# Kernel tuning notes

Hardware: AMD Instinct MI355X
Metric: run time of the kernel (lower is better)

Reference implementation:

```python
import jax, jax.numpy as jnp
import numpy as np

B, L, N, D, H, E = 16, 3, 512, 1024, 4096, 3


def setup_inputs() -> dict:
    key = jax.random.key(0)
    ks = jax.random.split(key, 6)
    tensors = jax.random.normal(ks[0], (B, L, N, D), jnp.float32)
    mask = jax.random.bernoulli(ks[1], 0.3, (B, L, N))  # True = padded
    wg = jax.random.normal(ks[2], (D, E), jnp.float32) * 0.02   # gate (Linear, no bias)
    We = jax.random.normal(ks[3], (E, D, D), jnp.float32) * 0.02  # per-expert Linear weight
    be = jnp.zeros((E, D), jnp.float32)                          # per-expert Linear bias
    Wp = jax.random.normal(ks[4], (D, H), jnp.float32) * 0.02    # GAP head projector
    bp = jnp.zeros((H,), jnp.float32)
    return dict(tensors=tensors, mask=mask, wg=wg, We=We, be=be, Wp=Wp, bp=bp)


def _moe_top1(x, wg, We, be):
    # x: [S, D]. DeepSpeed-style top-1 gating with capacity_factor=1.
    S, d = x.shape
    n_exp = wg.shape[1]
    cap = -(-S // n_exp)  # ceil(S / E) * capacity_factor(=1)
    gates = jax.nn.softmax(x @ wg, axis=-1)              # [S, E]
    idx = jnp.argmax(gates, axis=-1)                      # [S]
    m1 = jax.nn.one_hot(idx, n_exp, dtype=jnp.int32)      # [S, E]
    me = gates.mean(axis=0)
    ce = m1.astype(gates.dtype).mean(axis=0)
    l_aux = jnp.sum(me * ce) * n_exp                      # aux load-balancing loss
    # position of each token within its expert's buffer (arrival order)
    loc = jnp.cumsum(m1, axis=0) - 1                      # [S, E]
    loc_s = jnp.sum(loc * m1, axis=-1)                    # [S]
    keep = (loc_s < cap).astype(x.dtype)                  # drop overflow tokens
    gate_s = jnp.sum(gates * m1.astype(gates.dtype), axis=-1) * keep
    loc_c = jnp.minimum(loc_s, cap - 1)
    # dispatch (scatter), grouped GEMM per expert, combine (gather)
    disp = jnp.zeros((n_exp, cap, d), x.dtype).at[idx, loc_c].add(x * keep[:, None])
    eo = jnp.einsum('ecd,edh->ech', disp, We) + be[:, None, :]
    y = eo[idx, loc_c] * gate_s[:, None]                  # [S, D]
    return y, l_aux


def reference(tensors, mask, wg, We, be, Wp, bp):
    b, l, n, d = tensors.shape
    # permute(0,2,1,3).reshape(B*N, L, D) then flatten tokens
    x = tensors.transpose(0, 2, 1, 3).reshape(b * n * l, d)
    y, l_aux = _moe_top1(x, wg, We, be)
    y = y.reshape(b, n, l, d).transpose(0, 2, 1, 3)       # back to [B, L, N, D]
    # GAP head: projector then masked mean pool (sum over ALL tokens,
    # divided by non-masked count, matching the source exactly)
    p = y @ Wp + bp                                       # [B, L, N, H]
    p = p.reshape(b, l * n, -1)
    m = mask.reshape(b, l * n)
    s = p.sum(axis=1)                                     # [B, H]
    cnt = jnp.clip(jnp.sum(~m, axis=1, keepdims=True), 1, None).astype(p.dtype)
    return s / cnt, l_aux
```

## Files before the change

### kernel.cpp

```cpp
#include <hip/hip_runtime.h>
#include <hip/hip_bf16.h>
#include <cstdint>

#define LL 3
#define NN 512
#define DD 1024
#define HH 4096
#define SS 24576
#define LNTOK 1536
#define CAP 8192

#define OFF_HIST    0
#define OFF_GSUM    640
#define OFF_GBE     704
#define OFF_CNTI    768
#define OFF_NDROP   832
#define OFF_Z       960
#define OFF_YS      50112
#define OFF_ZEROEND 66496
#define OFF_IDX     66496
#define OFF_GVAL    91072
#define OFF_DROP    115648
#define OFF_END     132032
#define OFF_PZ      132032
#define OFF_PP      656320
#define OFF_YS2     1704896
#define OFF_BIG_END 1721280

__global__ __launch_bounds__(256) void k0_mask(const void* __restrict__ maskp,
                                               int* __restrict__ cnti) {
  __shared__ int det;
  __shared__ int scnt;
  int tid = threadIdx.x;
  if (tid == 0) { det = 0; scnt = 0; }
  __syncthreads();
  const uint32_t* mw = (const uint32_t*)maskp;
  for (int i = tid; i < LNTOK; i += 256) {
    uint32_t v = mw[i];
    if (v == 0x3F800000u) det = 2;
    else if (v > 1u) det = 1;
  }
  __syncthreads();
  int t = blockIdx.x * 256 + tid;
  int zero;
  if (det == 1) zero = (((const uint8_t*)maskp)[t] == 0);
  else          zero = (mw[t] == 0);
  unsigned long long bal = __ballot(zero);
  if ((tid & 63) == 0) atomicAdd(&scnt, __popcll(bal));
  __syncthreads();
  if (tid == 0) atomicAdd(&cnti[blockIdx.x / 6], scnt);
}

__global__ __launch_bounds__(256, 4) void k1_gate(const float* __restrict__ x,
                                                  const float* __restrict__ wg,
                                                  int* __restrict__ idx,
                                                  float* __restrict__ gval,
                                                  int* __restrict__ hist,
                                                  float* __restrict__ gsum,
                                                  float* __restrict__ gbe) {
  __shared__ float wgT[3][1024];
  __shared__ float part[16 * 195];
  __shared__ float sd[48];
  __shared__ float sG[3], sB[3];
  __shared__ int   sH[3];
  int tid = threadIdx.x, lane = tid & 63, w = tid >> 6;
  for (int i = tid; i < 3072; i += 256) wgT[i % 3][i / 3] = wg[i];
  if (tid < 3) { sG[tid] = 0.f; sB[tid] = 0.f; sH[tid] = 0; }
  __syncthreads();
  int dd = lane * 4;
  float4 W[12];
#pragma unroll
  for (int e = 0; e < 3; ++e)
#pragma unroll
    for (int q = 0; q < 4; ++q)
      W[e * 4 + q] = *(const float4*)(&wgT[e][dd + q * 256]);
  int t0 = blockIdx.x * 16;
  int b = t0 / LNTOK;
  int r0 = t0 % LNTOK;

#pragma unroll
  for (int k = 0; k < 4; ++k) {
    int tok = w * 4 + k;
    int r = r0 + tok;
    int n = r / LL, l = r % LL;
    const float* row = x + (size_t)((b * LL + l) * NN + n) * DD + dd;
    float4 v0 = *(const float4*)(row);
    float4 v1 = *(const float4*)(row + 256);
    float4 v2 = *(const float4*)(row + 512);
    float4 v3 = *(const float4*)(row + 768);
    float d0 = v0.x * W[0].x + v0.y * W[0].y + v0.z * W[0].z + v0.w * W[0].w +
               v1.x * W[1].x + v1.y * W[1].y + v1.z * W[1].z + v1.w * W[1].w +
               v2.x * W[2].x + v2.y * W[2].y + v2.z * W[2].z + v2.w * W[2].w +
               v3.x * W[3].x + v3.y * W[3].y + v3.z * W[3].z + v3.w * W[3].w;
    float d1 = v0.x * W[4].x + v0.y * W[4].y + v0.z * W[4].z + v0.w * W[4].w +
               v1.x * W[5].x + v1.y * W[5].y + v1.z * W[5].z + v1.w * W[5].w +
               v2.x * W[6].x + v2.y * W[6].y + v2.z * W[6].z + v2.w * W[6].w +
               v3.x * W[7].x + v3.y * W[7].y + v3.z * W[7].z + v3.w * W[7].w;
    float d2 = v0.x * W[8].x + v0.y * W[8].y + v0.z * W[8].z + v0.w * W[8].w +
               v1.x * W[9].x + v1.y * W[9].y + v1.z * W[9].z + v1.w * W[9].w +
               v2.x * W[10].x + v2.y * W[10].y + v2.z * W[10].z + v2.w * W[10].w +
               v3.x * W[11].x + v3.y * W[11].y + v3.z * W[11].z + v3.w * W[11].w;
    part[tok * 195 + lane] = d0;
    part[tok * 195 + 65 + lane] = d1;
    part[tok * 195 + 130 + lane] = d2;
  }
  __syncthreads();

  if (tid < 48) {
    const float* p = part + tid * 65;
    float s0 = 0, s1 = 0, s2 = 0, s3 = 0;
#pragma unroll
    for (int l = 0; l < 64; l += 4) {
      s0 += p[l]; s1 += p[l + 1]; s2 += p[l + 2]; s3 += p[l + 3];
    }
    sd[tid] = (s0 + s1) + (s2 + s3);
  }
  __syncthreads();

  if (tid < 16) {
    float d0 = sd[tid * 3], d1 = sd[tid * 3 + 1], d2 = sd[tid * 3 + 2];
    float m = d0; int id = 0;
    if (d1 > m) { m = d1; id = 1; }
    if (d2 > m) { m = d2; id = 2; }
    float e0 = expf(d0 - m), e1 = expf(d1 - m), e2 = expf(d2 - m);
    float inv = 1.0f / (e0 + e1 + e2);
    int t = t0 + tid;
    idx[t] = id;
    gval[t] = inv;
    atomicAdd(&sG[0], e0 * inv);
    atomicAdd(&sG[1], e1 * inv);
    atomicAdd(&sG[2], e2 * inv);
    atomicAdd(&sB[id], inv);
    atomicAdd(&sH[id], 1);
  }
  __syncthreads();
  if (tid < 3) {
    atomicAdd(&gsum[tid], sG[tid]);
    atomicAdd(&gbe[b * 3 + tid], sB[tid]);
    atomicAdd(&hist[(blockIdx.x >> 4) * 3 + tid], sH[tid]);
  }
}

__global__ __launch_bounds__(256, 4) void k2_zacc(const float* __restrict__ x,
                                                  const int* __restrict__ idx,
                                                  const float* __restrict__ gval,
                                                  float* __restrict__ z) {
  __shared__ float sg[384];
  __shared__ int   se[384];
  __shared__ float pacc[4][3][64];
  int tid = threadIdx.x;
  int blk = blockIdx.x;
  int b = blk >> 6, s = (blk >> 2) & 15, q = blk & 3;
  int tg = tid >> 6, ld = tid & 63;
  for (int i = tid; i < 384; i += 256) {
    int t = b * LNTOK + q * 384 + i;
    sg[i] = gval[t];
    se[i] = idx[t];
  }
  __syncthreads();
  float a0 = 0.f, a1 = 0.f, a2 = 0.f;
  int n0 = q * 128 + tg * 32;
  const float* xb = x + (size_t)b * LL * NN * DD + s * 64 + ld;
  int sb = tg * 96;
#pragma unroll 4
  for (int j = 0; j < 32; ++j) {
    int n = n0 + j;
#pragma unroll
    for (int l = 0; l < 3; ++l) {
      float v = xb[(size_t)(l * NN + n) * DD];
      int si = sb + j * 3 + l;
      float g = sg[si];
      int e = se[si];
      a0 += (e == 0) ? g * v : 0.f;
      a1 += (e == 1) ? g * v : 0.f;
      a2 += (e == 2) ? g * v : 0.f;
    }
  }
  pacc[tg][0][ld] = a0;
  pacc[tg][1][ld] = a1;
  pacc[tg][2][ld] = a2;
  __syncthreads();
  if (tid < 192) {
    int e = tid / 64, d = tid & 63;
    float ssum = (pacc[0][e][d] + pacc[1][e][d]) + (pacc[2][e][d] + pacc[3][e][d]);
    atomicAdd(&z[(size_t)b * 3072 + e * 1024 + s * 64 + d], ssum);
  }
}

__global__ __launch_bounds__(256) void k3a_drops(const int* __restrict__ idx,
                                                 const float* __restrict__ gval,
                                                 const int* __restrict__ hist,
                                                 const float* __restrict__ gsum,
                                                 float* __restrict__ gbe,
                                                 int* __restrict__ drop,
                                                 int* __restrict__ ndrop,
                                                 float* __restrict__ laux_out) {
  __shared__ int sh[288];
  __shared__ int scb[3];
  __shared__ int whist[4][3];
  int tid = threadIdx.x;
  for (int i = tid; i < 288; i += 256) sh[i] = hist[i];
  __syncthreads();
  if (tid < 3) {
    int s = 0;
    for (int c = 0; c < (int)blockIdx.x; ++c) s += sh[c * 3 + tid];
    scb[tid] = s;
  }
  __syncthreads();
  if (blockIdx.x == 95 && tid == 0) {
    int r0 = scb[0] + sh[285], r1 = scb[1] + sh[286], r2 = scb[2] + sh[287];
    float invS = 1.0f / (float)SS;
    *laux_out = 3.0f * (gsum[0] * invS * ((float)r0 * invS) +
                        gsum[1] * invS * ((float)r1 * invS) +
                        gsum[2] * invS * ((float)r2 * invS));
  }
  int cb0 = scb[0], cb1 = scb[1], cb2 = scb[2];
  if (cb0 <= CAP - 256 && cb1 <= CAP - 256 && cb2 <= CAP - 256) return;
  int t = blockIdx.x * 256 + tid;
  int e = idx[t];
  float gv = gval[t];
  int lane = tid & 63, w = tid >> 6;
  unsigned long long m0 = __ballot(e == 0);
  unsigned long long m1 = __ballot(e == 1);
  unsigned long long m2 = __ballot(e == 2);
  if (lane == 0) {
    whist[w][0] = __popcll(m0);
    whist[w][1] = __popcll(m1);
    whist[w][2] = __popcll(m2);
  }
  __syncthreads();
  int pre = 0;
  for (int ww = 0; ww < 3; ++ww)
    if (ww < w) pre += whist[ww][e];
  unsigned long long lt = (1ull << lane) - 1ull;
  unsigned long long me = (e == 0) ? m0 : (e == 1) ? m1 : m2;
  int cb = (e == 0) ? cb0 : (e == 1) ? cb1 : cb2;
  int pos = cb + pre + __popcll(me & lt);
  bool dropf = (pos >= CAP);
  unsigned long long db = __ballot(dropf);
  if (db) {
    int base = 0;
    if (lane == 0) base = atomicAdd(ndrop, __popcll(db));
    base = __shfl(base, 0);
    if (dropf) {
      int rank = __popcll(db & lt);
      int b = t / LNTOK;
      drop[base + rank] = t | (e << 20);
      atomicAdd(&gbe[b * 3 + e], -gv);
    }
  }
}

__global__ __launch_bounds__(256) void k3b_sub(const float* __restrict__ x,
                                               const float* __restrict__ gval,
                                               const int* __restrict__ drop,
                                               const int* __restrict__ ndrop,
                                               float* __restrict__ z) {
  int nd = *ndrop;
  for (int i = blockIdx.x; i < nd; i += gridDim.x) {
    int ent = drop[i];
    int t = ent & 0xFFFFF;
    int e = ent >> 20;
    int b = t / LNTOK;
    int r = t % LNTOK;
    int n = r / LL, l = r % LL;
    float g = gval[t];
    const float* row = x + (size_t)((b * LL + l) * NN + n) * DD;
    float* zr = z + (size_t)b * 3072 + e * 1024;
    int d = threadIdx.x * 4;
    float4 v = *(const float4*)(row + d);
    atomicAdd(&zr[d + 0], -g * v.x);
    atomicAdd(&zr[d + 1], -g * v.y);
    atomicAdd(&zr[d + 2], -g * v.z);
    atomicAdd(&zr[d + 3], -g * v.w);
  }
}

__global__ __launch_bounds__(256) void k4_we(const float* __restrict__ z,
                                             const float* __restrict__ We,
                                             float* __restrict__ pz) {
  __shared__ float ztT[96][20];
  __shared__ float pacc[4][16][64];
  int tid = threadIdx.x;
  int nt = blockIdx.x & 15, kc = blockIdx.x >> 4;
  int n0 = nt * 64, k0 = kc * 96;
  for (int i = tid; i < 1536; i += 256) {
    int m = i / 96, kk = i % 96;
    ztT[kk][m] = z[m * 3072 + k0 + kk];
  }
  __syncthreads();
  int kg = tid >> 6, n = tid & 63;
  float acc[16];
#pragma unroll
  for (int m = 0; m < 16; ++m) acc[m] = 0.f;
  const float* wp = We + (size_t)(k0 + kg * 24) * 1024 + n0 + n;
#pragma unroll
  for (int kk = 0; kk < 24; ++kk) {
    float bw = wp[(size_t)kk * 1024];
    int k = kg * 24 + kk;
    const float4 y0 = *(const float4*)(&ztT[k][0]);
    const float4 y1 = *(const float4*)(&ztT[k][4]);
    const float4 y2 = *(const float4*)(&ztT[k][8]);
    const float4 y3 = *(const float4*)(&ztT[k][12]);
    acc[0] += y0.x * bw;  acc[1] += y0.y * bw;  acc[2] += y0.z * bw;  acc[3] += y0.w * bw;
    acc[4] += y1.x * bw;  acc[5] += y1.y * bw;  acc[6] += y1.z * bw;  acc[7] += y1.w * bw;
    acc[8] += y2.x * bw;  acc[9] += y2.y * bw;  acc[10] += y2.z * bw; acc[11] += y2.w * bw;
    acc[12] += y3.x * bw; acc[13] += y3.y * bw; acc[14] += y3.z * bw; acc[15] += y3.w * bw;
  }
#pragma unroll
  for (int m = 0; m < 16; ++m) pacc[kg][m][n] = acc[m];
  __syncthreads();
  for (int i = tid; i < 1024; i += 256) {
    int m = i >> 6, nn = i & 63;
    float s = (pacc[0][m][nn] + pacc[1][m][nn]) + (pacc[2][m][nn] + pacc[3][m][nn]);
    pz[((size_t)kc * 16 + m) * 1024 + n0 + nn] = s;
  }
}

__global__ __launch_bounds__(256) void k4r_red(const float* __restrict__ pz,
                                               const float* __restrict__ gbe,
                                               const float* __restrict__ be,
                                               float* __restrict__ ys2) {
  int i = blockIdx.x * 256 + threadIdx.x;
  int m = i >> 10, k = i & 1023;
  float s = 0.f;
#pragma unroll 8
  for (int kc = 0; kc < 32; ++kc) s += pz[((size_t)kc * 16 + m) * 1024 + k];
  s += gbe[m * 3 + 0] * be[k] + gbe[m * 3 + 1] * be[1024 + k] +
       gbe[m * 3 + 2] * be[2048 + k];
  ys2[i] = s;
}

__global__ __launch_bounds__(256) void k5_wp(const float* __restrict__ ys2,
                                             const float* __restrict__ Wp,
                                             float* __restrict__ pp) {
  __shared__ float ytT[64][20];
  __shared__ float pacc[4][16][64];
  int tid = threadIdx.x;
  int ht = blockIdx.x & 63, kc = blockIdx.x >> 6;
  int h0 = ht * 64, k0 = kc * 64;
  for (int i = tid; i < 1024; i += 256) {
    int m = i >> 6, kk = i & 63;
    ytT[kk][m] = ys2[m * 1024 + k0 + kk];
  }
  __syncthreads();
  int kg = tid >> 6, h = tid & 63;
  float acc[16];
#pragma unroll
  for (int m = 0; m < 16; ++m) acc[m] = 0.f;
  const float* wpp = Wp + (size_t)(k0 + kg * 16) * HH + h0 + h;
#pragma unroll
  for (int kk = 0; kk < 16; ++kk) {
    float bw = wpp[(size_t)kk * HH];
    int k = kg * 16 + kk;
    const float4 y0 = *(const float4*)(&ytT[k][0]);
    const float4 y1 = *(const float4*)(&ytT[k][4]);
    const float4 y2 = *(const float4*)(&ytT[k][8]);
    const float4 y3 = *(const float4*)(&ytT[k][12]);
    acc[0] += y0.x * bw;  acc[1] += y0.y * bw;  acc[2] += y0.z * bw;  acc[3] += y0.w * bw;
    acc[4] += y1.x * bw;  acc[5] += y1.y * bw;  acc[6] += y1.z * bw;  acc[7] += y1.w * bw;
    acc[8] += y2.x * bw;  acc[9] += y2.y * bw;  acc[10] += y2.z * bw; acc[11] += y2.w * bw;
    acc[12] += y3.x * bw; acc[13] += y3.y * bw; acc[14] += y3.z * bw; acc[15] += y3.w * bw;
  }
#pragma unroll
  for (int m = 0; m < 16; ++m) pacc[kg][m][h] = acc[m];
  __syncthreads();
  for (int i = tid; i < 1024; i += 256) {
    int m = i >> 6, hh = i & 63;
    float s = (pacc[0][m][hh] + pacc[1][m][hh]) + (pacc[2][m][hh] + pacc[3][m][hh]);
    pp[((size_t)kc * 16 + m) * HH + h0 + hh] = s;
  }
}

__global__ __launch_bounds__(256) void k5r_red(const float* __restrict__ pp,
                                               const float* __restrict__ bp,
                                               const int* __restrict__ cnti,
                                               float* __restrict__ out) {
  int i = blockIdx.x * 256 + threadIdx.x;
  int m = i >> 12, h = i & 4095;
  float s = 0.f;
#pragma unroll 8
  for (int kc = 0; kc < 16; ++kc) s += pp[((size_t)kc * 16 + m) * HH + h];
  float inv = 1.0f / fmaxf(1.0f, (float)cnti[m]);
  out[i] = (s + 1536.0f * bp[h]) * inv;
}

__global__ __launch_bounds__(256) void k4_we_at(const float* __restrict__ z,
                                                const float* __restrict__ We,
                                                float* __restrict__ ys) {
  __shared__ float zt[16][64];
  __shared__ float Ct[16][128];
  int tid = threadIdx.x;
  int nt = blockIdx.x & 7, ks = blockIdx.x >> 3;
  int n0 = nt * 128, k0 = ks * 64;
  for (int i = tid; i < 1024; i += 256)
    zt[i >> 6][i & 63] = z[(i >> 6) * 3072 + k0 + (i & 63)];
  for (int i = tid; i < 2048; i += 256) ((float*)Ct)[i] = 0.f;
  __syncthreads();
  int c4 = (tid & 31) * 4;
  int kg = tid >> 5;
  float4 acc[16];
#pragma unroll
  for (int m = 0; m < 16; ++m) acc[m] = make_float4(0.f, 0.f, 0.f, 0.f);
  const float* wp = We + (size_t)(k0 + kg * 8) * 1024 + n0 + c4;
#pragma unroll
  for (int kk = 0; kk < 8; ++kk) {
    float4 bv = *(const float4*)(wp + (size_t)kk * 1024);
#pragma unroll
    for (int m = 0; m < 16; ++m) {
      float a = zt[m][kg * 8 + kk];
      acc[m].x += a * bv.x; acc[m].y += a * bv.y;
      acc[m].z += a * bv.z; acc[m].w += a * bv.w;
    }
  }
#pragma unroll
  for (int m = 0; m < 16; ++m) {
    atomicAdd(&Ct[m][c4 + 0], acc[m].x);
    atomicAdd(&Ct[m][c4 + 1], acc[m].y);
    atomicAdd(&Ct[m][c4 + 2], acc[m].z);
    atomicAdd(&Ct[m][c4 + 3], acc[m].w);
  }
  __syncthreads();
  for (int i = tid; i < 2048; i += 256) {
    int m = i >> 7;
    int h = ((i & 127) + ks * 8) & 127;
    atomicAdd(&ys[m * 1024 + n0 + h], Ct[m][h]);
  }
}

__global__ __launch_bounds__(256) void k5_out_at(const float* __restrict__ ys,
                                                 const float* __restrict__ Wp,
                                                 const float* __restrict__ be,
                                                 const float* __restrict__ gbe,
                                                 const float* __restrict__ bp,
                                                 const int* __restrict__ cnti,
                                                 float* __restrict__ out) {
  __shared__ float ytT[1024][16];
  __shared__ float Ct[16][64];
  __shared__ float sgbe[48];
  __shared__ float sinv[16];
  int tid = threadIdx.x;
  int n0 = blockIdx.x * 64;
  if (tid < 48) sgbe[tid] = gbe[tid];
  if (tid < 16) sinv[tid] = 1.0f / fmaxf(1.0f, (float)cnti[tid]);
  for (int i = tid; i < 1024; i += 256) ((float*)Ct)[i] = 0.f;
  __syncthreads();
  for (int i = tid; i < 16384; i += 256) {
    int m = i >> 10, k = i & 1023;
    ytT[k][m] = ys[m * 1024 + k] + sgbe[m * 3 + 0] * be[k] +
                sgbe[m * 3 + 1] * be[1024 + k] + sgbe[m * 3 + 2] * be[2048 + k];
  }
  __syncthreads();
  int kg = tid >> 4, nl = tid & 15;
  int h0 = nl * 4;
  float4 acc[16];
#pragma unroll
  for (int m = 0; m < 16; ++m) acc[m] = make_float4(0.f, 0.f, 0.f, 0.f);
  const float* wpp = Wp + (size_t)(kg * 64) * HH + n0 + h0;
  for (int kk = 0; kk < 64; ++kk) {
    int k = kg * 64 + kk;
    float4 bv = *(const float4*)(wpp + (size_t)kk * HH);
    const float4 y0 = *(const float4*)(&ytT[k][0]);
    const float4 y1 = *(const float4*)(&ytT[k][4]);
    const float4 y2 = *(const float4*)(&ytT[k][8]);
    const float4 y3 = *(const float4*)(&ytT[k][12]);
    acc[0].x += y0.x * bv.x;  acc[0].y += y0.x * bv.y;  acc[0].z += y0.x * bv.z;  acc[0].w += y0.x * bv.w;
    acc[1].x += y0.y * bv.x;  acc[1].y += y0.y * bv.y;  acc[1].z += y0.y * bv.z;  acc[1].w += y0.y * bv.w;
    acc[2].x += y0.z * bv.x;  acc[2].y += y0.z * bv.y;  acc[2].z += y0.z * bv.z;  acc[2].w += y0.z * bv.w;
    acc[3].x += y0.w * bv.x;  acc[3].y += y0.w * bv.y;  acc[3].z += y0.w * bv.z;  acc[3].w += y0.w * bv.w;
    acc[4].x += y1.x * bv.x;  acc[4].y += y1.x * bv.y;  acc[4].z += y1.x * bv.z;  acc[4].w += y1.x * bv.w;
    acc[5].x += y1.y * bv.x;  acc[5].y += y1.y * bv.y;  acc[5].z += y1.y * bv.z;  acc[5].w += y1.y * bv.w;
    acc[6].x += y1.z * bv.x;  acc[6].y += y1.z * bv.y;  acc[6].z += y1.z * bv.z;  acc[6].w += y1.z * bv.w;
    acc[7].x += y1.w * bv.x;  acc[7].y += y1.w * bv.y;  acc[7].z += y1.w * bv.z;  acc[7].w += y1.w * bv.w;
    acc[8].x += y2.x * bv.x;  acc[8].y += y2.x * bv.y;  acc[8].z += y2.x * bv.z;  acc[8].w += y2.x * bv.w;
    acc[9].x += y2.y * bv.x;  acc[9].y += y2.y * bv.y;  acc[9].z += y2.y * bv.z;  acc[9].w += y2.y * bv.w;
    acc[10].x += y2.z * bv.x; acc[10].y += y2.z * bv.y; acc[10].z += y2.z * bv.z; acc[10].w += y2.z * bv.w;
    acc[11].x += y2.w * bv.x; acc[11].y += y2.w * bv.y; acc[11].z += y2.w * bv.z; acc[11].w += y2.w * bv.w;
    acc[12].x += y3.x * bv.x; acc[12].y += y3.x * bv.y; acc[12].z += y3.x * bv.z; acc[12].w += y3.x * bv.w;
    acc[13].x += y3.y * bv.x; acc[13].y += y3.y * bv.y; acc[13].z += y3.y * bv.z; acc[13].w += y3.y * bv.w;
    acc[14].x += y3.z * bv.x; acc[14].y += y3.z * bv.y; acc[14].z += y3.z * bv.z; acc[14].w += y3.z * bv.w;
    acc[15].x += y3.w * bv.x; acc[15].y += y3.w * bv.y; acc[15].z += y3.w * bv.z; acc[15].w += y3.w * bv.w;
  }
#pragma unroll
  for (int m = 0; m < 16; ++m) {
    atomicAdd(&Ct[m][h0 + 0], acc[m].x);
    atomicAdd(&Ct[m][h0 + 1], acc[m].y);
    atomicAdd(&Ct[m][h0 + 2], acc[m].z);
    atomicAdd(&Ct[m][h0 + 3], acc[m].w);
  }
  __syncthreads();
  for (int i = tid; i < 1024; i += 256) {
    int m = i >> 6, h = i & 63;
    out[(size_t)m * HH + n0 + h] = (Ct[m][h] + 1536.0f * bp[n0 + h]) * sinv[m];
  }
}

extern "C" void kernel_launch(void* const* d_in, const int* in_sizes, int n_in,
                              void* d_out, int out_size, void* d_ws, size_t ws_size,
                              hipStream_t stream) {
  const float* x    = (const float*)d_in[0];
  const void*  mask = d_in[1];
  const float* wg   = (const float*)d_in[2];
  const float* We   = (const float*)d_in[3];
  const float* be   = (const float*)d_in[4];
  const float* Wp   = (const float*)d_in[5];
  const float* bp   = (const float*)d_in[6];
  float* out = (float*)d_out;
  float* wsf = (float*)d_ws;
  int*   wsi = (int*)d_ws;
  bool big = ws_size >= (size_t)OFF_BIG_END * 4;

  hipMemsetAsync(d_ws, 0, (size_t)OFF_ZEROEND * 4, stream);

  k0_mask<<<96, 256, 0, stream>>>(mask, wsi + OFF_CNTI);
  k1_gate<<<1536, 256, 0, stream>>>(x, wg, wsi + OFF_IDX, wsf + OFF_GVAL,
                                    wsi + OFF_HIST, wsf + OFF_GSUM,
                                    wsf + OFF_GBE);
  k2_zacc<<<1024, 256, 0, stream>>>(x, wsi + OFF_IDX, wsf + OFF_GVAL,
                                    wsf + OFF_Z);
  k3a_drops<<<96, 256, 0, stream>>>(wsi + OFF_IDX, wsf + OFF_GVAL,
                                    wsi + OFF_HIST, wsf + OFF_GSUM,
                                    wsf + OFF_GBE, wsi + OFF_DROP,
                                    wsi + OFF_NDROP, out + 65536);
  k3b_sub<<<128, 256, 0, stream>>>(x, wsf + OFF_GVAL, wsi + OFF_DROP,
                                   wsi + OFF_NDROP, wsf + OFF_Z);
  if (big) {
    k4_we<<<512, 256, 0, stream>>>(wsf + OFF_Z, We, wsf + OFF_PZ);
    k4r_red<<<64, 256, 0, stream>>>(wsf + OFF_PZ, wsf + OFF_GBE, be,
                                    wsf + OFF_YS2);
    k5_wp<<<1024, 256, 0, stream>>>(wsf + OFF_YS2, Wp, wsf + OFF_PP);
    k5r_red<<<256, 256, 0, stream>>>(wsf + OFF_PP, bp, wsi + OFF_CNTI, out);
  } else {
    k4_we_at<<<384, 256, 0, stream>>>(wsf + OFF_Z, We, wsf + OFF_YS);
    k5_out_at<<<64, 256, 0, stream>>>(wsf + OFF_YS, Wp, be, wsf + OFF_GBE, bp,
                                      wsi + OFF_CNTI, out);
  }
}
```

Before: 108.3 us.

## Fuse mask count and drop subtraction into one drops kernel, coarsen gate/zacc

Removes the separate mask-count kernel and the drop-subtraction kernel by folding both into a single per-chunk drops kernel that collects dropped tokens in shared memory and subtracts them directly. The gate kernel now handles 32 tokens per block. The z-accumulation kernel uses 512-thread blocks covering a full batch, so it stores its results instead of using atomics, which also lets the memset skip zeroing the z region on the big path. This cuts launch count and atomic traffic, at the cost of fewer blocks in the gate and zacc kernels and a serial per-block loop over dropped tokens.

```diff
diff --git a/kernel.cpp b/kernel.cpp
--- a/kernel.cpp
+++ b/kernel.cpp
@@ -14,42 +14,17 @@
 #define OFF_GSUM    640
 #define OFF_GBE     704
 #define OFF_CNTI    768
-#define OFF_NDROP   832
+#define OFF_SCALEND 960
 #define OFF_Z       960
 #define OFF_YS      50112
 #define OFF_ZEROEND 66496
 #define OFF_IDX     66496
 #define OFF_GVAL    91072
-#define OFF_DROP    115648
 #define OFF_END     132032
 #define OFF_PZ      132032
 #define OFF_PP      656320
 #define OFF_YS2     1704896
 #define OFF_BIG_END 1721280
-
-__global__ __launch_bounds__(256) void k0_mask(const void* __restrict__ maskp,
-                                               int* __restrict__ cnti) {
-  __shared__ int det;
-  __shared__ int scnt;
-  int tid = threadIdx.x;
-  if (tid == 0) { det = 0; scnt = 0; }
-  __syncthreads();
-  const uint32_t* mw = (const uint32_t*)maskp;
-  for (int i = tid; i < LNTOK; i += 256) {
-    uint32_t v = mw[i];
-    if (v == 0x3F800000u) det = 2;
-    else if (v > 1u) det = 1;
-  }
-  __syncthreads();
-  int t = blockIdx.x * 256 + tid;
-  int zero;
-  if (det == 1) zero = (((const uint8_t*)maskp)[t] == 0);
-  else          zero = (mw[t] == 0);
-  unsigned long long bal = __ballot(zero);
-  if ((tid & 63) == 0) atomicAdd(&scnt, __popcll(bal));
-  __syncthreads();
-  if (tid == 0) atomicAdd(&cnti[blockIdx.x / 6], scnt);
-}
 
 __global__ __launch_bounds__(256, 4) void k1_gate(const float* __restrict__ x,
                                                   const float* __restrict__ wg,
@@ -59,8 +34,8 @@
                                                   float* __restrict__ gsum,
                                                   float* __restrict__ gbe) {
   __shared__ float wgT[3][1024];
-  __shared__ float part[16 * 195];
-  __shared__ float sd[48];
+  __shared__ float part[32 * 195];
+  __shared__ float sd[96];
   __shared__ float sG[3], sB[3];
   __shared__ int   sH[3];
   int tid = threadIdx.x, lane = tid & 63, w = tid >> 6;
@@ -74,13 +49,13 @@
 #pragma unroll
     for (int q = 0; q < 4; ++q)
       W[e * 4 + q] = *(const float4*)(&wgT[e][dd + q * 256]);
-  int t0 = blockIdx.x * 16;
+  int t0 = blockIdx.x * 32;
   int b = t0 / LNTOK;
   int r0 = t0 % LNTOK;
 
 #pragma unroll
-  for (int k = 0; k < 4; ++k) {
-    int tok = w * 4 + k;
+  for (int k = 0; k < 8; ++k) {
+    int tok = w * 8 + k;
     int r = r0 + tok;
     int n = r / LL, l = r % LL;
     const float* row = x + (size_t)((b * LL + l) * NN + n) * DD + dd;
@@ -106,7 +81,7 @@
   }
   __syncthreads();
 
-  if (tid < 48) {
+  if (tid < 96) {
     const float* p = part + tid * 65;
     float s0 = 0, s1 = 0, s2 = 0, s3 = 0;
 #pragma unroll
@@ -117,7 +92,7 @@
   }
   __syncthreads();
 
-  if (tid < 16) {
+  if (tid < 32) {
     float d0 = sd[tid * 3], d1 = sd[tid * 3 + 1], d2 = sd[tid * 3 + 2];
     float m = d0; int id = 0;
     if (d1 > m) { m = d1; id = 1; }
@@ -137,38 +112,36 @@
   if (tid < 3) {
     atomicAdd(&gsum[tid], sG[tid]);
     atomicAdd(&gbe[b * 3 + tid], sB[tid]);
-    atomicAdd(&hist[(blockIdx.x >> 4) * 3 + tid], sH[tid]);
-  }
-}
-
-__global__ __launch_bounds__(256, 4) void k2_zacc(const float* __restrict__ x,
-                                                  const int* __restrict__ idx,
-                                                  const float* __restrict__ gval,
-                                                  float* __restrict__ z) {
-  __shared__ float sg[384];
-  __shared__ int   se[384];
-  __shared__ float pacc[4][3][64];
+    atomicAdd(&hist[(blockIdx.x >> 3) * 3 + tid], sH[tid]);
+  }
+}
+
+__global__ __launch_bounds__(512) void k2_zacc(const float* __restrict__ x,
+                                               const int* __restrict__ idx,
+                                               const float* __restrict__ gval,
+                                               float* __restrict__ z) {
+  __shared__ float sg[1536];
+  __shared__ int   se[1536];
+  __shared__ float pacc[8][3][64];
   int tid = threadIdx.x;
-  int blk = blockIdx.x;
-  int b = blk >> 6, s = (blk >> 2) & 15, q = blk & 3;
+  int b = blockIdx.x >> 4, s = blockIdx.x & 15;
   int tg = tid >> 6, ld = tid & 63;
-  for (int i = tid; i < 384; i += 256) {
-    int t = b * LNTOK + q * 384 + i;
+  for (int i = tid; i < 1536; i += 512) {
+    int t = b * LNTOK + i;
     sg[i] = gval[t];
     se[i] = idx[t];
   }
   __syncthreads();
   float a0 = 0.f, a1 = 0.f, a2 = 0.f;
-  int n0 = q * 128 + tg * 32;
   const float* xb = x + (size_t)b * LL * NN * DD + s * 64 + ld;
-  int sb = tg * 96;
+  int nbase = tg * 64;
 #pragma unroll 4
-  for (int j = 0; j < 32; ++j) {
-    int n = n0 + j;
+  for (int j = 0; j < 64; ++j) {
+    int n = nbase + j;
 #pragma unroll
     for (int l = 0; l < 3; ++l) {
       float v = xb[(size_t)(l * NN + n) * DD];
-      int si = sb + j * 3 + l;
+      int si = n * 3 + l;
       float g = sg[si];
       int e = se[si];
       a0 += (e == 0) ? g * v : 0.f;
@@ -182,32 +155,58 @@
   __syncthreads();
   if (tid < 192) {
     int e = tid / 64, d = tid & 63;
-    float ssum = (pacc[0][e][d] + pacc[1][e][d]) + (pacc[2][e][d] + pacc[3][e][d]);
-    atomicAdd(&z[(size_t)b * 3072 + e * 1024 + s * 64 + d], ssum);
-  }
-}
-
-__global__ __launch_bounds__(256) void k3a_drops(const int* __restrict__ idx,
-                                                 const float* __restrict__ gval,
-                                                 const int* __restrict__ hist,
-                                                 const float* __restrict__ gsum,
-                                                 float* __restrict__ gbe,
-                                                 int* __restrict__ drop,
-                                                 int* __restrict__ ndrop,
-                                                 float* __restrict__ laux_out) {
+    float s8 = 0.f;
+#pragma unroll
+    for (int g = 0; g < 8; ++g) s8 += pacc[g][e][d];
+    z[(size_t)b * 3072 + e * 1024 + s * 64 + d] = s8;
+  }
+}
+
+__global__ __launch_bounds__(256) void k3_drops(const float* __restrict__ x,
+                                                const int* __restrict__ idx,
+                                                const float* __restrict__ gval,
+                                                const int* __restrict__ hist,
+                                                const float* __restrict__ gsum,
+                                                const void* __restrict__ maskp,
+                                                float* __restrict__ gbe,
+                                                float* __restrict__ z,
+                                                int* __restrict__ cnti,
+                                                float* __restrict__ laux_out) {
   __shared__ int sh[288];
   __shared__ int scb[3];
   __shared__ int whist[4][3];
+  __shared__ int det, scnt, dcnt;
+  __shared__ int   dtok[256];
+  __shared__ float dg[256];
   int tid = threadIdx.x;
+  int c = blockIdx.x;
+  int b = c / 6;
+  if (tid == 0) { det = 0; scnt = 0; dcnt = 0; }
   for (int i = tid; i < 288; i += 256) sh[i] = hist[i];
   __syncthreads();
+  const uint32_t* mw = (const uint32_t*)maskp;
+  for (int i = tid; i < LNTOK; i += 256) {
+    uint32_t v = mw[i];
+    if (v == 0x3F800000u) det = 2;
+    else if (v > 1u) det = 1;
+  }
   if (tid < 3) {
     int s = 0;
-    for (int c = 0; c < (int)blockIdx.x; ++c) s += sh[c * 3 + tid];
+    for (int cc = 0; cc < c; ++cc) s += sh[cc * 3 + tid];
     scb[tid] = s;
   }
   __syncthreads();
-  if (blockIdx.x == 95 && tid == 0) {
+  {
+    int tmask = c * 256 + tid;
+    int zero;
+    if (det == 1) zero = (((const uint8_t*)maskp)[tmask] == 0);
+    else          zero = (mw[tmask] == 0);
+    unsigned long long bal = __ballot(zero);
+    if ((tid & 63) == 0) atomicAdd(&scnt, __popcll(bal));
+  }
+  __syncthreads();
+  if (tid == 0) atomicAdd(&cnti[b], scnt);
+  if (c == 95 && tid == 0) {
     int r0 = scb[0] + sh[285], r1 = scb[1] + sh[286], r2 = scb[2] + sh[287];
     float invS = 1.0f / (float)SS;
     *laux_out = 3.0f * (gsum[0] * invS * ((float)r0 * invS) +
@@ -216,7 +215,7 @@
   }
   int cb0 = scb[0], cb1 = scb[1], cb2 = scb[2];
   if (cb0 <= CAP - 256 && cb1 <= CAP - 256 && cb2 <= CAP - 256) return;
-  int t = blockIdx.x * 256 + tid;
+  int t = c * 256 + tid;
   int e = idx[t];
   float gv = gval[t];
   int lane = tid & 63, w = tid >> 6;
@@ -236,43 +235,29 @@
   unsigned long long me = (e == 0) ? m0 : (e == 1) ? m1 : m2;
   int cb = (e == 0) ? cb0 : (e == 1) ? cb1 : cb2;
   int pos = cb + pre + __popcll(me & lt);
-  bool dropf = (pos >= CAP);
-  unsigned long long db = __ballot(dropf);
-  if (db) {
-    int base = 0;
-    if (lane == 0) base = atomicAdd(ndrop, __popcll(db));
-    base = __shfl(base, 0);
-    if (dropf) {
-      int rank = __popcll(db & lt);
-      int b = t / LNTOK;
-      drop[base + rank] = t | (e << 20);
-      atomicAdd(&gbe[b * 3 + e], -gv);
-    }
-  }
-}
-
-__global__ __launch_bounds__(256) void k3b_sub(const float* __restrict__ x,
-                                               const float* __restrict__ gval,
-                                               const int* __restrict__ drop,
-                                               const int* __restrict__ ndrop,
-                                               float* __restrict__ z) {
-  int nd = *ndrop;
-  for (int i = blockIdx.x; i < nd; i += gridDim.x) {
-    int ent = drop[i];
-    int t = ent & 0xFFFFF;
-    int e = ent >> 20;
-    int b = t / LNTOK;
-    int r = t % LNTOK;
+  if (pos >= CAP) {
+    int slot = atomicAdd(&dcnt, 1);
+    dtok[slot] = tid | (e << 16);
+    dg[slot] = gv;
+    atomicAdd(&gbe[b * 3 + e], -gv);
+  }
+  __syncthreads();
+  int nd = dcnt;
+  float* zb = z + (size_t)b * 3072;
+  int d4 = tid * 4;
+  for (int i = 0; i < nd; ++i) {
+    int ent = dtok[i];
+    int tok = ent & 0xFFFF, te = ent >> 16;
+    float g = dg[i];
+    int r = (c * 256 + tok) % LNTOK;
     int n = r / LL, l = r % LL;
-    float g = gval[t];
     const float* row = x + (size_t)((b * LL + l) * NN + n) * DD;
-    float* zr = z + (size_t)b * 3072 + e * 1024;
-    int d = threadIdx.x * 4;
-    float4 v = *(const float4*)(row + d);
-    atomicAdd(&zr[d + 0], -g * v.x);
-    atomicAdd(&zr[d + 1], -g * v.y);
-    atomicAdd(&zr[d + 2], -g * v.z);
-    atomicAdd(&zr[d + 3], -g * v.w);
+    float4 v = *(const float4*)(row + d4);
+    float* zr = zb + te * 1024 + d4;
+    atomicAdd(&zr[0], -g * v.x);
+    atomicAdd(&zr[1], -g * v.y);
+    atomicAdd(&zr[2], -g * v.z);
+    atomicAdd(&zr[3], -g * v.w);
   }
 }
 
@@ -510,20 +495,18 @@
   int*   wsi = (int*)d_ws;
   bool big = ws_size >= (size_t)OFF_BIG_END * 4;
 
-  hipMemsetAsync(d_ws, 0, (size_t)OFF_ZEROEND * 4, stream);
-
-  k0_mask<<<96, 256, 0, stream>>>(mask, wsi + OFF_CNTI);
-  k1_gate<<<1536, 256, 0, stream>>>(x, wg, wsi + OFF_IDX, wsf + OFF_GVAL,
-                                    wsi + OFF_HIST, wsf + OFF_GSUM,
-                                    wsf + OFF_GBE);
-  k2_zacc<<<1024, 256, 0, stream>>>(x, wsi + OFF_IDX, wsf + OFF_GVAL,
-                                    wsf + OFF_Z);
-  k3a_drops<<<96, 256, 0, stream>>>(wsi + OFF_IDX, wsf + OFF_GVAL,
-                                    wsi + OFF_HIST, wsf + OFF_GSUM,
-                                    wsf + OFF_GBE, wsi + OFF_DROP,
-                                    wsi + OFF_NDROP, out + 65536);
-  k3b_sub<<<128, 256, 0, stream>>>(x, wsf + OFF_GVAL, wsi + OFF_DROP,
-                                   wsi + OFF_NDROP, wsf + OFF_Z);
+  hipMemsetAsync(d_ws, 0,
+                 (size_t)(big ? OFF_SCALEND : OFF_ZEROEND) * 4, stream);
+
+  k1_gate<<<768, 256, 0, stream>>>(x, wg, wsi + OFF_IDX, wsf + OFF_GVAL,
+                                   wsi + OFF_HIST, wsf + OFF_GSUM,
+                                   wsf + OFF_GBE);
+  k2_zacc<<<256, 512, 0, stream>>>(x, wsi + OFF_IDX, wsf + OFF_GVAL,
+                                   wsf + OFF_Z);
+  k3_drops<<<96, 256, 0, stream>>>(x, wsi + OFF_IDX, wsf + OFF_GVAL,
+                                   wsi + OFF_HIST, wsf + OFF_GSUM, mask,
+                                   wsf + OFF_GBE, wsf + OFF_Z,
+                                   wsi + OFF_CNTI, out + 65536);
   if (big) {
     k4_we<<<512, 256, 0, stream>>>(wsf + OFF_Z, We, wsf + OFF_PZ);
     k4r_red<<<64, 256, 0, stream>>>(wsf + OFF_PZ, wsf + OFF_GBE, be,
```

New measurement: 133.4 us. 1.23x slower.
